# Kernel optimization log

Hardware: AMD Instinct MI355X
Metric: run time of the kernel (lower is better)

## Reference

```python
import jax, jax.numpy as jnp
import numpy as np

B, N, P, H, E, M, O, T = 4, 128, 512, 64, 32, 64, 64, 64

def _normalize(v, axis=-1, eps=1e-12):
    n = jnp.sqrt(jnp.sum(v * v, axis=axis, keepdims=True))
    return v / jnp.maximum(n, eps)

def _quat_mul(a, b):
    aw, ax, ay, az = a[..., 0], a[..., 1], a[..., 2], a[..., 3]
    bw, bx, by, bz = b[..., 0], b[..., 1], b[..., 2], b[..., 3]
    return jnp.stack([
        aw*bw - ax*bx - ay*by - az*bz,
        aw*bx + ax*bw + ay*bz - az*by,
        aw*by - ax*bz + ay*bw + az*bx,
        aw*bz + ax*by - ay*bx + az*bw], axis=-1)

def _quat_conj(q):
    return q * jnp.array([1.0, -1.0, -1.0, -1.0], dtype=q.dtype)

def _quat_rotate(q, v):
    # rotate vectors v [...,3] by unit quaternions q [...,4] in (w,x,y,z)
    qv = q[..., 1:]
    w = q[..., :1]
    t = 2.0 * jnp.cross(qv, v)
    return v + w * t + jnp.cross(qv, t)

def _mlp(x, W1, b1, W2, b2):
    return jax.nn.relu(x @ W1 + b1) @ W2 + b2

def setup_inputs():
    key = jax.random.key(0)
    ks = jax.random.split(key, 20)
    def w(k, i, o):
        return (jax.random.normal(k, (i, o), jnp.float32) / np.sqrt(i)).astype(jnp.float32)
    inp = dict(
        q=_normalize(jax.random.normal(ks[0], (B, N, 4), jnp.float32)),
        x=jax.random.normal(ks[1], (B, N, 3), jnp.float32),
        torsions=jax.random.normal(ks[2], (B, N, 7, 2), jnp.float32),
        h=jax.random.normal(ks[3], (B, N, H), jnp.float32),
        e=jax.random.normal(ks[4], (B, N, N, E), jnp.float32),
        node_mask=jnp.ones((B, N), bool),
        pocket_q=_normalize(jax.random.normal(ks[5], (B, P, 4), jnp.float32)),
        pocket_x=jax.random.normal(ks[6], (B, P, 3), jnp.float32),
        pocket_e=jax.random.normal(ks[7], (B, N, P, E), jnp.float32),
        pocket_h=jax.random.normal(ks[8], (B, P, H), jnp.float32),
        pocket_mask=jnp.ones((B, P), bool),
        Wm1=w(ks[9], 2 * H + E + 9, T), bm1=jnp.zeros((T,), jnp.float32),
        Wm2=w(ks[10], T, M), bm2=jnp.zeros((M,), jnp.float32),
        Wf1=w(ks[11], H + M, T), bf1=jnp.zeros((T,), jnp.float32),
        Wf2=w(ks[12], T, O), bf2=jnp.zeros((O,), jnp.float32),
        Wx1=w(ks[13], M, T), bx1=jnp.zeros((T,), jnp.float32),
        Wx2=w(ks[14], T, 3), bx2=jnp.zeros((3,), jnp.float32),
        Wq1=w(ks[15], M, T), bq1=jnp.zeros((T,), jnp.float32),
        Wq2=w(ks[16], T, 4), bq2=jnp.zeros((4,), jnp.float32),
        Wt1=w(ks[17], M, T), bt1=jnp.zeros((T,), jnp.float32),
        Wt2=w(ks[18], T, 14), bt2=jnp.zeros((14,), jnp.float32),
    )
    return inp

def _forward(q, x, torsions, h, e, pocket_q, pocket_x, pocket_e, pocket_h,
             node_mask, pocket_mask,
             Wm1, bm1, Wm2, bm2, Wf1, bf1, Wf2, bf2,
             Wx1, bx1, Wx2, bx2, Wq1, bq1, Wq2, bq2, Wt1, bt1, Wt2, bt2):
    b, n, hd = h.shape
    p = pocket_h.shape[-2]
    eye = jnp.eye(n, dtype=bool)
    pep_mm = node_mask[:, :, None] & node_mask[:, None, :] & (~eye)[None]
    poc_mm = node_mask[:, :, None] & pocket_mask[:, None, :]
    msg_mask = jnp.concatenate([pep_mm, poc_mm], axis=-1).astype(h.dtype)  # [B,N,N+P]
    n_neigh = (node_mask.sum(-1) + pocket_mask.sum(-1) - 1).astype(h.dtype)

    all_x = jnp.concatenate([x, pocket_x], axis=-2)   # [B,N+P,3]
    all_q = jnp.concatenate([q, pocket_q], axis=-2)   # [B,N+P,4]

    diff = x[:, :, None, :] - all_x[:, None, :, :]    # [B,N,N+P,3]
    d2 = jnp.sum(diff * diff, axis=-1)                # [B,N,N+P] == cat(peptide_d2, pocket_d2)
    qdot = jnp.abs(jnp.sum(q[:, :, None, :] * all_q[:, None, :, :], axis=-1))
    conj_j = _quat_conj(all_q)[:, None, :, :]         # inverse of frame j rotation
    local_x = _quat_rotate(conj_j, diff)              # R_j^T (x_i - x_j): global_to_local.apply
    local_q = _quat_mul(conj_j, q[:, :, None, :])     # q_j^{-1} * q_i

    hi = jnp.broadcast_to(h[:, :, None, :], (b, n, n + p, hd))
    hj = jnp.broadcast_to(jnp.concatenate([h, pocket_h], axis=-2)[:, None, :, :], (b, n, n + p, hd))
    e_all = jnp.concatenate([e, pocket_e], axis=-2)

    feat = jnp.concatenate([hi, hj, e_all, local_x, local_q, d2[..., None], qdot[..., None]], axis=-1)
    m = _mlp(feat, Wm1, bm1, Wm2, bm2) * msg_mask[..., None]
    msum = m.sum(axis=-2)                             # [B,N,M]

    o = _mlp(jnp.concatenate([h, msum], axis=-1), Wf1, bf1, Wf2, bf2)
    upd_torsions = _normalize(_mlp(msum, Wt1, bt1, Wt2, bt2).reshape(torsions.shape))

    dx = _mlp(m, Wx1, bx1, Wx2, bx2) * msg_mask[..., None]
    dq = _mlp(msum, Wq1, bq1, Wq2, bq2)
    ident = jnp.array([1.0, 0.0, 0.0, 0.0], dtype=dq.dtype)
    dq = jnp.where(node_mask[..., None], dq, ident)
    dq = _normalize(dq)
    upd_q = _quat_mul(q, dq)
    upd_q = jnp.where(node_mask[..., None], upd_q, ident)
    upd_q = _normalize(upd_q)                         # Rigid(Rotation(..., normalize_quats=True))

    rot_j = _normalize(all_q)[:, None, :, :]          # local->global rotation, normalize_quats=True
    upd_x = x + _quat_rotate(rot_j, dx).sum(axis=-2) / n_neigh[:, None, None]
    return upd_q, upd_x, upd_torsions, o

def reference(q, x, torsions, h, e, node_mask, pocket_q, pocket_x, pocket_e, pocket_h, pocket_mask,
              Wm1, bm1, Wm2, bm2, Wf1, bf1, Wf2, bf2,
              Wx1, bx1, Wx2, bx2, Wq1, bq1, Wq2, bq2, Wt1, bt1, Wt2, bt2):
    return _forward(q, x, torsions, h, e, pocket_q, pocket_x, pocket_e, pocket_h,
                    node_mask, pocket_mask,
                    Wm1, bm1, Wm2, bm2, Wf1, bf1, Wf2, bf2,
                    Wx1, bx1, Wx2, bx2, Wq1, bq1, Wq2, bq2, Wt1, bt1, Wt2, bt2)
```

## Files before the change

### kernel.cpp

```cpp
#include <hip/hip_runtime.h>
#include <stdint.h>

#define NB 4
#define NN 128
#define NP 512
#define NJ 640
#define HD 64
#define ED 32
#define NW 8

typedef unsigned short u16;
typedef __attribute__((ext_vector_type(8))) short short8;
typedef __attribute__((ext_vector_type(4))) float f32x4;

#define OFF_Q 0
#define OFF_X 2048
#define OFF_T 3584
#define OFF_O 10752

__device__ __forceinline__ uint32_t cvtpk(float a, float b) {
  uint32_t r;
  asm("v_cvt_pk_bf16_f32 %0, %1, %2" : "=v"(r) : "v"(a), "v"(b));
  return r;
}
__device__ __forceinline__ u16 bfh(float a) { return (u16)cvtpk(a, 0.f); }

__device__ __forceinline__ int w1row64(int k) {
  if (k < 32) return 128 + k;
  if (k < 35) return 160 + (k - 32);
  if (k < 39) return 163 + (k - 35);
  if (k == 39) return 167;
  if (k == 40) return 168;
  return -1;
}

__global__ void __launch_bounds__(256)
hj_pre(const float* __restrict__ h, const float* __restrict__ ph,
       const float* __restrict__ Wm1, float* __restrict__ HjW) {
  const int r = blockIdx.x * 4 + (threadIdx.x >> 6);
  const int lane = threadIdx.x & 63;
  const int b = r / NJ, j = r - b * NJ;
  const float* hr = (j < NN) ? h + ((size_t)(b * NN + j)) * HD
                             : ph + ((size_t)(b * NP + (j - NN))) * HD;
  float hv = hr[lane];
  float acc = 0.f;
#pragma unroll 16
  for (int k = 0; k < 64; ++k)
    acc += __shfl(hv, k) * Wm1[(size_t)(64 + k) * 64 + lane];
  HjW[(size_t)r * 64 + lane] = acc;
}

__global__ void __launch_bounds__(512, 2)
egnn_fused(const float* __restrict__ q, const float* __restrict__ x,
           const float* __restrict__ h, const float* __restrict__ e,
           const float* __restrict__ pe, const float* __restrict__ pq,
           const float* __restrict__ px, const float* __restrict__ ph,
           const float* __restrict__ HjW,
           const float* __restrict__ Wm1, const float* __restrict__ bm1,
           const float* __restrict__ Wm2, const float* __restrict__ bm2,
           const float* __restrict__ Wx1, const float* __restrict__ bx1,
           const float* __restrict__ Wx2, const float* __restrict__ bx2,
           const float* __restrict__ Wf1, const float* __restrict__ bf1,
           const float* __restrict__ Wf2, const float* __restrict__ bf2_,
           const float* __restrict__ Wq1, const float* __restrict__ bq1,
           const float* __restrict__ Wq2, const float* __restrict__ bq2,
           const float* __restrict__ Wt1, const float* __restrict__ bt1,
           const float* __restrict__ Wt2, const float* __restrict__ bt2,
           float* __restrict__ out)
{
  __shared__ __align__(16) u16 sW1B[64 * 64];
  __shared__ __align__(16) u16 sW2B[64 * 64];
  __shared__ __align__(16) u16 sWx1B[64 * 64];
  __shared__ __align__(16) u16 sWx2B[16 * 64];
  __shared__ __align__(16) u16 sF[NW][16 * 64];
  __shared__ __align__(16) u16 sT[NW][16 * 64];
  __shared__ float sDxT[NW][16][3];
  __shared__ float sMsum[NW][64];
  __shared__ float sDx[NW][3];
  __shared__ float sHiP[64];

  const int b = blockIdx.x >> 7;
  const int i = blockIdx.x & 127;
  const int tid = threadIdx.x;
  const int wid = tid >> 6;
  const int lane = tid & 63;
  const int nl = lane & 15;
  const int quad = lane >> 4;
  const size_t node = (size_t)(b * NN + i);

  u16* sFw = sF[wid];
  u16* sTw = sT[wid];

  const int er = lane >> 2, ec = lane & 3;

  float4 EA, EB;
  {
    int jr = wid * 16 + er;
    const float* eb = (jr < NN)
        ? e + ((node * NN) + jr) * ED + ec * 8
        : pe + ((node * NP) + (jr - NN)) * ED + ec * 8;
    EA = *(const float4*)eb;
    EB = *(const float4*)(eb + 4);
  }

  for (int idx = tid; idx < 64 * 64; idx += 512) {
    int n = idx >> 6, k = idx & 63;
    int ks = k ^ ((n & 7) << 3);
    int row = w1row64(k);
    sW1B[n * 64 + ks]  = (row < 0) ? (u16)0 : bfh(Wm1[(size_t)row * 64 + n]);
    sW2B[n * 64 + ks]  = bfh(Wm2[(size_t)k * 64 + n]);
    sWx1B[n * 64 + ks] = bfh(Wx1[(size_t)k * 64 + n]);
  }
  for (int idx = tid; idx < 16 * 64; idx += 512) {
    int n = idx >> 6, k = idx & 63;
    sWx2B[n * 64 + (k ^ ((n & 7) << 3))] =
        (n < 3) ? bfh(Wx2[(size_t)k * 3 + n]) : (u16)0;
  }
  for (int idx = lane; idx < 16 * 64 / 2; idx += 64) ((uint32_t*)sFw)[idx] = 0;

  if (tid >= 64 && tid < 128) {
    int col = tid - 64;
    float acc = bm1[col];
#pragma unroll 8
    for (int k = 0; k < HD; ++k) acc += h[node * HD + k] * Wm1[k * 64 + col];
    sHiP[col] = acc;
  }

  const float* qr0 = q + node * 4;
  const float qi0 = qr0[0], qi1 = qr0[1], qi2 = qr0[2], qi3 = qr0[3];
  const float* xr0 = x + node * 3;
  const float xi0 = xr0[0], xi1 = xr0[1], xi2 = xr0[2];

  __syncthreads();

  float HiF[4], bm2F[4], bx1F[4];
#pragma unroll
  for (int nt = 0; nt < 4; ++nt) {
    HiF[nt] = sHiP[nt * 16 + nl];
    bm2F[nt] = bm2[nt * 16 + nl];
    bx1F[nt] = bx1[nt * 16 + nl];
  }
  const float bx2F = (nl < 3) ? bx2[nl] : 0.f;

  f32x4 msum[4];
#pragma unroll
  for (int nt = 0; nt < 4; ++nt) msum[nt] = (f32x4){0.f, 0.f, 0.f, 0.f};
  float dxs0 = 0.f, dxs1 = 0.f, dxs2 = 0.f;

  const int swr = (nl & 7) << 3;
  const float* HjB = HjW + (size_t)b * NJ * 64;

  for (int tl = wid; tl < 40; tl += NW) {
    const int jb = tl * 16;

    float hj[4][4];
#pragma unroll
    for (int r = 0; r < 4; ++r)
#pragma unroll
      for (int nt = 0; nt < 4; ++nt)
        hj[r][nt] = HjB[(size_t)(jb + quad * 4 + r) * 64 + nt * 16 + nl];

    float4 qj;
    float xj0 = 0.f, xj1 = 0.f, xj2 = 0.f;
    if (lane < 16) {
      int j = jb + lane;
      const float* qr = (j < NN) ? q + ((size_t)(b * NN + j)) * 4
                                 : pq + ((size_t)(b * NP + (j - NN))) * 4;
      qj = *(const float4*)qr;
      const float* xr = (j < NN) ? x + ((size_t)(b * NN + j)) * 3
                                 : px + ((size_t)(b * NP + (j - NN))) * 3;
      xj0 = xr[0]; xj1 = xr[1]; xj2 = xr[2];
    }

    {
      const int sw = (er & 7) << 3;
      uint4 pw;
      pw.x = cvtpk(EA.x, EA.y); pw.y = cvtpk(EA.z, EA.w);
      pw.z = cvtpk(EB.x, EB.y); pw.w = cvtpk(EB.z, EB.w);
      *(uint4*)&sFw[er * 64 + ((ec * 8) ^ sw)] = pw;
    }
    if (tl + NW < 40) {
      int jr2 = (tl + NW) * 16 + er;
      const float* eb = (jr2 < NN)
          ? e + ((node * NN) + jr2) * ED + ec * 8
          : pe + ((node * NP) + (jr2 - NN)) * ED + ec * 8;
      EA = *(const float4*)eb;
      EB = *(const float4*)(eb + 4);
    }

    float nqw = 0.f, nqx = 0.f, nqy = 0.f, nqz = 0.f;
    if (lane < 16) {
      float d0 = xi0 - xj0, d1 = xi1 - xj1, d2v = xi2 - xj2;
      float d2 = d0 * d0 + d1 * d1 + d2v * d2v;
      float qdot = fabsf(qi0 * qj.x + qi1 * qj.y + qi2 * qj.z + qi3 * qj.w);
      float ajw = qj.x, ajx = -qj.y, ajy = -qj.z, ajz = -qj.w;
      float t0 = 2.f * (ajy * d2v - ajz * d1);
      float t1 = 2.f * (ajz * d0 - ajx * d2v);
      float t2 = 2.f * (ajx * d1 - ajy * d0);
      float lx0 = d0 + ajw * t0 + (ajy * t2 - ajz * t1);
      float lx1 = d1 + ajw * t1 + (ajz * t0 - ajx * t2);
      float lx2 = d2v + ajw * t2 + (ajx * t1 - ajy * t0);
      float lqw = ajw * qi0 - ajx * qi1 - ajy * qi2 - ajz * qi3;
      float lqx = ajw * qi1 + ajx * qi0 + ajy * qi3 - ajz * qi2;
      float lqy = ajw * qi2 - ajx * qi3 + ajy * qi0 + ajz * qi1;
      float lqz = ajw * qi3 + ajx * qi2 - ajy * qi1 + ajz * qi0;
      float nn2 = qj.x * qj.x + qj.y * qj.y + qj.z * qj.z + qj.w * qj.w;
      float rn = 1.f / fmaxf(sqrtf(nn2), 1e-12f);
      nqw = qj.x * rn; nqx = qj.y * rn; nqy = qj.z * rn; nqz = qj.w * rn;
      uint4 g0, g1;
      g0.x = cvtpk(lx0, lx1); g0.y = cvtpk(lx2, lqw);
      g0.z = cvtpk(lqx, lqy); g0.w = cvtpk(lqz, d2);
      g1.x = cvtpk(qdot, 0.f); g1.y = 0; g1.z = 0; g1.w = 0;
      const int sw = (lane & 7) << 3;
      *(uint4*)&sFw[lane * 64 + (32 ^ sw)] = g0;
      *(uint4*)&sFw[lane * 64 + (40 ^ sw)] = g1;
    }

    f32x4 acc[4];
#pragma unroll
    for (int nt = 0; nt < 4; ++nt)
      acc[nt] = (f32x4){HiF[nt] + hj[0][nt], HiF[nt] + hj[1][nt],
                        HiF[nt] + hj[2][nt], HiF[nt] + hj[3][nt]};
#pragma unroll
    for (int ks = 0; ks < 2; ++ks) {
      const int ko = (ks * 32 + quad * 8) ^ swr;
      short8 af = *(const short8*)&sFw[nl * 64 + ko];
#pragma unroll
      for (int nt = 0; nt < 4; ++nt) {
        short8 bfr = *(const short8*)&sW1B[(nt * 16 + nl) * 64 + ko];
        acc[nt] = __builtin_amdgcn_mfma_f32_16x16x32_bf16(af, bfr, acc[nt], 0, 0, 0);
      }
    }
#pragma unroll
    for (int r = 0; r < 4; ++r) {
      const int row = quad * 4 + r;
      const int sw2 = (row & 7) << 3;
#pragma unroll
      for (int nt = 0; nt < 4; ++nt)
        sTw[row * 64 + ((nt * 16 + nl) ^ sw2)] = bfh(fmaxf(acc[nt][r], 0.f));
    }

#pragma unroll
    for (int nt = 0; nt < 4; ++nt)
      acc[nt] = (f32x4){bm2F[nt], bm2F[nt], bm2F[nt], bm2F[nt]};
#pragma unroll
    for (int ks = 0; ks < 2; ++ks) {
      const int ko = (ks * 32 + quad * 8) ^ swr;
      short8 af = *(const short8*)&sTw[nl * 64 + ko];
#pragma unroll
      for (int nt = 0; nt < 4; ++nt) {
        short8 bfr = *(const short8*)&sW2B[(nt * 16 + nl) * 64 + ko];
        acc[nt] = __builtin_amdgcn_mfma_f32_16x16x32_bf16(af, bfr, acc[nt], 0, 0, 0);
      }
    }
#pragma unroll
    for (int r = 0; r < 4; ++r) {
      const int row = quad * 4 + r;
      const int sw2 = (row & 7) << 3;
#pragma unroll
      for (int nt = 0; nt < 4; ++nt) {
        float v = acc[nt][r];
        if (jb + row == i) v = 0.f;
        msum[nt][r] += v;
        sTw[row * 64 + ((nt * 16 + nl) ^ sw2)] = bfh(v);
      }
    }

#pragma unroll
    for (int nt = 0; nt < 4; ++nt)
      acc[nt] = (f32x4){bx1F[nt], bx1F[nt], bx1F[nt], bx1F[nt]};
#pragma unroll
    for (int ks = 0; ks < 2; ++ks) {
      const int ko = (ks * 32 + quad * 8) ^ swr;
      short8 af = *(const short8*)&sTw[nl * 64 + ko];
#pragma unroll
      for (int nt = 0; nt < 4; ++nt) {
        short8 bfr = *(const short8*)&sWx1B[(nt * 16 + nl) * 64 + ko];
        acc[nt] = __builtin_amdgcn_mfma_f32_16x16x32_bf16(af, bfr, acc[nt], 0, 0, 0);
      }
    }
#pragma unroll
    for (int r = 0; r < 4; ++r) {
      const int row = quad * 4 + r;
      const int sw2 = (row & 7) << 3;
#pragma unroll
      for (int nt = 0; nt < 4; ++nt)
        sTw[row * 64 + ((nt * 16 + nl) ^ sw2)] = bfh(fmaxf(acc[nt][r], 0.f));
    }

    f32x4 dacc = (f32x4){bx2F, bx2F, bx2F, bx2F};
#pragma unroll
    for (int ks = 0; ks < 2; ++ks) {
      const int ko = (ks * 32 + quad * 8) ^ swr;
      short8 af = *(const short8*)&sTw[nl * 64 + ko];
      short8 bfr = *(const short8*)&sWx2B[nl * 64 + ko];
      dacc = __builtin_amdgcn_mfma_f32_16x16x32_bf16(af, bfr, dacc, 0, 0, 0);
    }
    if (nl < 3) {
#pragma unroll
      for (int r = 0; r < 4; ++r) sDxT[wid][quad * 4 + r][nl] = dacc[r];
    }
    if (lane < 16) {
      int j = jb + lane;
      if (j != i) {
        float dxc0 = sDxT[wid][lane][0];
        float dxc1 = sDxT[wid][lane][1];
        float dxc2 = sDxT[wid][lane][2];
        float rt0 = 2.f * (nqy * dxc2 - nqz * dxc1);
        float rt1 = 2.f * (nqz * dxc0 - nqx * dxc2);
        float rt2 = 2.f * (nqx * dxc1 - nqy * dxc0);
        dxs0 += dxc0 + nqw * rt0 + (nqy * rt2 - nqz * rt1);
        dxs1 += dxc1 + nqw * rt1 + (nqz * rt0 - nqx * rt2);
        dxs2 += dxc2 + nqw * rt2 + (nqx * rt1 - nqy * rt0);
      }
    }
  }

#pragma unroll
  for (int nt = 0; nt < 4; ++nt) {
    float s = msum[nt][0] + msum[nt][1] + msum[nt][2] + msum[nt][3];
    s += __shfl_xor(s, 16);
    s += __shfl_xor(s, 32);
    if (lane < 16) sMsum[wid][nt * 16 + lane] = s;
  }
  {
    float a = dxs0, bb = dxs1, cc = dxs2;
#pragma unroll
    for (int off = 1; off < 16; off <<= 1) {
      a += __shfl_xor(a, off);
      bb += __shfl_xor(bb, off);
      cc += __shfl_xor(cc, off);
    }
    if (lane == 0) { sDx[wid][0] = a; sDx[wid][1] = bb; sDx[wid][2] = cc; }
  }
  __syncthreads();

  float* sPh3 = (float*)sWx2B;
  if (wid == 0) {
    float ms = 0.f;
#pragma unroll
    for (int w = 0; w < NW; ++w) ms += sMsum[w][lane];
    sPh3[0 * 64 + lane] = ms;
    float f1a = bf1[lane], f1b = 0.f;
    __syncwarp();
#pragma unroll 8
    for (int k = 0; k < 64; ++k) {
      f1a += h[node * HD + k] * Wf1[k * 64 + lane];
      f1b += sPh3[0 * 64 + k] * Wf1[(64 + k) * 64 + lane];
    }
    float f1 = fmaxf(f1a + f1b, 0.f);
    __syncwarp();
    sPh3[0 * 64 + lane] = f1;
    float oacc = bf2_[lane];
    __syncwarp();
#pragma unroll 8
    for (int k = 0; k < 64; ++k) oacc += sPh3[0 * 64 + k] * Wf2[k * 64 + lane];
    out[OFF_O + node * 64 + lane] = oacc;
  } else if (wid == 1) {
    float ms = 0.f;
#pragma unroll
    for (int w = 0; w < NW; ++w) ms += sMsum[w][lane];
    sPh3[1 * 64 + lane] = ms;
    float a = bq1[lane];
    __syncwarp();
#pragma unroll 8
    for (int k = 0; k < 64; ++k) a += sPh3[1 * 64 + k] * Wq1[k * 64 + lane];
    a = fmaxf(a, 0.f);
    float p0 = a * Wq2[lane * 4 + 0];
    float p1 = a * Wq2[lane * 4 + 1];
    float p2 = a * Wq2[lane * 4 + 2];
    float p3 = a * Wq2[lane * 4 + 3];
#pragma unroll
    for (int off = 32; off >= 1; off >>= 1) {
      p0 += __shfl_xor(p0, off);
      p1 += __shfl_xor(p1, off);
      p2 += __shfl_xor(p2, off);
      p3 += __shfl_xor(p3, off);
    }
    float dq0 = p0 + bq2[0], dq1 = p1 + bq2[1];
    float dq2 = p2 + bq2[2], dq3 = p3 + bq2[3];
    float n = fmaxf(sqrtf(dq0 * dq0 + dq1 * dq1 + dq2 * dq2 + dq3 * dq3), 1e-12f);
    dq0 /= n; dq1 /= n; dq2 /= n; dq3 /= n;
    float uw = qi0 * dq0 - qi1 * dq1 - qi2 * dq2 - qi3 * dq3;
    float ux = qi0 * dq1 + qi1 * dq0 + qi2 * dq3 - qi3 * dq2;
    float uy = qi0 * dq2 - qi1 * dq3 + qi2 * dq0 + qi3 * dq1;
    float uz = qi0 * dq3 + qi1 * dq2 - qi2 * dq1 + qi3 * dq0;
    float n2 = fmaxf(sqrtf(uw * uw + ux * ux + uy * uy + uz * uz), 1e-12f);
    if (lane == 0) {
      float* po = out + OFF_Q + node * 4;
      po[0] = uw / n2; po[1] = ux / n2; po[2] = uy / n2; po[3] = uz / n2;
    }
  } else if (wid == 2) {
    float ms = 0.f;
#pragma unroll
    for (int w = 0; w < NW; ++w) ms += sMsum[w][lane];
    sPh3[2 * 64 + lane] = ms;
    float a = bt1[lane];
    __syncwarp();
#pragma unroll 8
    for (int k = 0; k < 64; ++k) a += sPh3[2 * 64 + k] * Wt1[k * 64 + lane];
    a = fmaxf(a, 0.f);
    __syncwarp();
    sPh3[2 * 64 + lane] = a;
    __syncwarp();
    if (lane < 14) {
      float v = bt2[lane];
#pragma unroll 8
      for (int k = 0; k < 64; ++k) v += sPh3[2 * 64 + k] * Wt2[k * 14 + lane];
      float pv = __shfl_xor(v, 1);
      float nrm = fmaxf(sqrtf(v * v + pv * pv), 1e-12f);
      out[OFF_T + node * 14 + lane] = v / nrm;
    }
  } else if (wid == 3) {
    if (lane < 3) {
      float xs = 0.f;
#pragma unroll
      for (int w = 0; w < NW; ++w) xs += sDx[w][lane];
      float xiv = (lane == 0) ? xi0 : (lane == 1) ? xi1 : xi2;
      out[OFF_X + node * 3 + lane] = xiv + xs / 639.0f;
    }
  }
}

extern "C" void kernel_launch(void* const* d_in, const int* in_sizes, int n_in,
                              void* d_out, int out_size, void* d_ws, size_t ws_size,
                              hipStream_t stream) {
  const float* q   = (const float*)d_in[0];
  const float* x   = (const float*)d_in[1];
  const float* h   = (const float*)d_in[3];
  const float* e   = (const float*)d_in[4];
  const float* pq  = (const float*)d_in[6];
  const float* px  = (const float*)d_in[7];
  const float* pe  = (const float*)d_in[8];
  const float* ph  = (const float*)d_in[9];
  const float* Wm1 = (const float*)d_in[11];
  const float* bm1 = (const float*)d_in[12];
  const float* Wm2 = (const float*)d_in[13];
  const float* bm2 = (const float*)d_in[14];
  const float* Wf1 = (const float*)d_in[15];
  const float* bf1 = (const float*)d_in[16];
  const float* Wf2 = (const float*)d_in[17];
  const float* bf2_ = (const float*)d_in[18];
  const float* Wx1 = (const float*)d_in[19];
  const float* bx1 = (const float*)d_in[20];
  const float* Wx2 = (const float*)d_in[21];
  const float* bx2 = (const float*)d_in[22];
  const float* Wq1 = (const float*)d_in[23];
  const float* bq1 = (const float*)d_in[24];
  const float* Wq2 = (const float*)d_in[25];
  const float* bq2 = (const float*)d_in[26];
  const float* Wt1 = (const float*)d_in[27];
  const float* bt1 = (const float*)d_in[28];
  const float* Wt2 = (const float*)d_in[29];
  const float* bt2 = (const float*)d_in[30];

  float* HjW = (float*)d_ws;

  hj_pre<<<NB * NJ / 4, 256, 0, stream>>>(h, ph, Wm1, HjW);
  egnn_fused<<<NB * NN, 512, 0, stream>>>(
      q, x, h, e, pe, pq, px, ph, HjW,
      Wm1, bm1, Wm2, bm2, Wx1, bx1, Wx2, bx2,
      Wf1, bf1, Wf2, bf2_, Wq1, bq1, Wq2, bq2,
      Wt1, bt1, Wt2, bt2, (float*)d_out);
}
```

Baseline: 190.4 us.

## Shrink shared memory and retile HjW layout to raise occupancy to four blocks

Merges the per-warp feature and temp LDS buffers into one, keeps Wx2 as register fragments instead of shared memory, and aliases the dx and message-sum scratch, so that four 512-thread blocks can share a CU (launch bounds raised from 2 to 4). The HjW precompute is written in a tiled, transposed layout so each lane can fetch its hj values with four float4 loads instead of sixteen scalar loads. The cost is tighter register limits under the new launch bound, with a risk of spills, and more reuse of a single LDS buffer across consecutive stages within a warp.

```diff
diff --git a/kernel.cpp b/kernel.cpp
--- a/kernel.cpp
+++ b/kernel.cpp
@@ -47,10 +47,10 @@
 #pragma unroll 16
   for (int k = 0; k < 64; ++k)
     acc += __shfl(hv, k) * Wm1[(size_t)(64 + k) * 64 + lane];
-  HjW[(size_t)r * 64 + lane] = acc;
+  HjW[((size_t)(b * 40 + (j >> 4))) * 1024 + lane * 16 + (j & 15)] = acc;
 }
 
-__global__ void __launch_bounds__(512, 2)
+__global__ void __launch_bounds__(512, 4)
 egnn_fused(const float* __restrict__ q, const float* __restrict__ x,
            const float* __restrict__ h, const float* __restrict__ e,
            const float* __restrict__ pe, const float* __restrict__ pq,
@@ -71,11 +71,8 @@
   __shared__ __align__(16) u16 sW1B[64 * 64];
   __shared__ __align__(16) u16 sW2B[64 * 64];
   __shared__ __align__(16) u16 sWx1B[64 * 64];
-  __shared__ __align__(16) u16 sWx2B[16 * 64];
-  __shared__ __align__(16) u16 sF[NW][16 * 64];
-  __shared__ __align__(16) u16 sT[NW][16 * 64];
-  __shared__ float sDxT[NW][16][3];
-  __shared__ float sMsum[NW][64];
+  __shared__ __align__(16) u16 sB[NW][16 * 64];
+  __shared__ float sRed[NW][64];
   __shared__ float sDx[NW][3];
   __shared__ float sHiP[64];
 
@@ -88,8 +85,8 @@
   const int quad = lane >> 4;
   const size_t node = (size_t)(b * NN + i);
 
-  u16* sFw = sF[wid];
-  u16* sTw = sT[wid];
+  u16* sBw = sB[wid];
+  float* sDxTw = sRed[wid];
 
   const int er = lane >> 2, ec = lane & 3;
 
@@ -111,12 +108,7 @@
     sW2B[n * 64 + ks]  = bfh(Wm2[(size_t)k * 64 + n]);
     sWx1B[n * 64 + ks] = bfh(Wx1[(size_t)k * 64 + n]);
   }
-  for (int idx = tid; idx < 16 * 64; idx += 512) {
-    int n = idx >> 6, k = idx & 63;
-    sWx2B[n * 64 + (k ^ ((n & 7) << 3))] =
-        (n < 3) ? bfh(Wx2[(size_t)k * 3 + n]) : (u16)0;
-  }
-  for (int idx = lane; idx < 16 * 64 / 2; idx += 64) ((uint32_t*)sFw)[idx] = 0;
+  for (int idx = lane; idx < 16 * 64 / 2; idx += 64) ((uint32_t*)sBw)[idx] = 0;
 
   if (tid >= 64 && tid < 128) {
     int col = tid - 64;
@@ -131,6 +123,19 @@
   const float* xr0 = x + node * 3;
   const float xi0 = xr0[0], xi1 = xr0[1], xi2 = xr0[2];
 
+  short8 Wx2f[2];
+#pragma unroll
+  for (int ks = 0; ks < 2; ++ks) {
+    const int k0 = ks * 32 + quad * 8;
+    float v[8];
+#pragma unroll
+    for (int r = 0; r < 8; ++r) v[r] = (nl < 3) ? Wx2[(size_t)(k0 + r) * 3 + nl] : 0.f;
+    union { uint32_t u[4]; short8 s; } cv;
+    cv.u[0] = cvtpk(v[0], v[1]); cv.u[1] = cvtpk(v[2], v[3]);
+    cv.u[2] = cvtpk(v[4], v[5]); cv.u[3] = cvtpk(v[6], v[7]);
+    Wx2f[ks] = cv.s;
+  }
+
   __syncthreads();
 
   float HiF[4], bm2F[4], bx1F[4];
@@ -148,17 +153,15 @@
   float dxs0 = 0.f, dxs1 = 0.f, dxs2 = 0.f;
 
   const int swr = (nl & 7) << 3;
-  const float* HjB = HjW + (size_t)b * NJ * 64;
 
   for (int tl = wid; tl < 40; tl += NW) {
     const int jb = tl * 16;
 
-    float hj[4][4];
-#pragma unroll
-    for (int r = 0; r < 4; ++r)
-#pragma unroll
-      for (int nt = 0; nt < 4; ++nt)
-        hj[r][nt] = HjB[(size_t)(jb + quad * 4 + r) * 64 + nt * 16 + nl];
+    const float* HjT = HjW + ((size_t)(b * 40 + tl)) * 1024;
+    float4 hjv[4];
+#pragma unroll
+    for (int nt = 0; nt < 4; ++nt)
+      hjv[nt] = *(const float4*)&HjT[(nt * 16 + nl) * 16 + quad * 4];
 
     float4 qj;
     float xj0 = 0.f, xj1 = 0.f, xj2 = 0.f;
@@ -177,7 +180,7 @@
       uint4 pw;
       pw.x = cvtpk(EA.x, EA.y); pw.y = cvtpk(EA.z, EA.w);
       pw.z = cvtpk(EB.x, EB.y); pw.w = cvtpk(EB.z, EB.w);
-      *(uint4*)&sFw[er * 64 + ((ec * 8) ^ sw)] = pw;
+      *(uint4*)&sBw[er * 64 + ((ec * 8) ^ sw)] = pw;
     }
     if (tl + NW < 40) {
       int jr2 = (tl + NW) * 16 + er;
@@ -212,19 +215,19 @@
       g0.z = cvtpk(lqx, lqy); g0.w = cvtpk(lqz, d2);
       g1.x = cvtpk(qdot, 0.f); g1.y = 0; g1.z = 0; g1.w = 0;
       const int sw = (lane & 7) << 3;
-      *(uint4*)&sFw[lane * 64 + (32 ^ sw)] = g0;
-      *(uint4*)&sFw[lane * 64 + (40 ^ sw)] = g1;
+      *(uint4*)&sBw[lane * 64 + (32 ^ sw)] = g0;
+      *(uint4*)&sBw[lane * 64 + (40 ^ sw)] = g1;
     }
 
     f32x4 acc[4];
 #pragma unroll
     for (int nt = 0; nt < 4; ++nt)
-      acc[nt] = (f32x4){HiF[nt] + hj[0][nt], HiF[nt] + hj[1][nt],
-                        HiF[nt] + hj[2][nt], HiF[nt] + hj[3][nt]};
+      acc[nt] = (f32x4){HiF[nt] + hjv[nt].x, HiF[nt] + hjv[nt].y,
+                        HiF[nt] + hjv[nt].z, HiF[nt] + hjv[nt].w};
 #pragma unroll
     for (int ks = 0; ks < 2; ++ks) {
       const int ko = (ks * 32 + quad * 8) ^ swr;
-      short8 af = *(const short8*)&sFw[nl * 64 + ko];
+      short8 af = *(const short8*)&sBw[nl * 64 + ko];
 #pragma unroll
       for (int nt = 0; nt < 4; ++nt) {
         short8 bfr = *(const short8*)&sW1B[(nt * 16 + nl) * 64 + ko];
@@ -237,7 +240,7 @@
       const int sw2 = (row & 7) << 3;
 #pragma unroll
       for (int nt = 0; nt < 4; ++nt)
-        sTw[row * 64 + ((nt * 16 + nl) ^ sw2)] = bfh(fmaxf(acc[nt][r], 0.f));
+        sBw[row * 64 + ((nt * 16 + nl) ^ sw2)] = bfh(fmaxf(acc[nt][r], 0.f));
     }
 
 #pragma unroll
@@ -246,7 +249,7 @@
 #pragma unroll
     for (int ks = 0; ks < 2; ++ks) {
       const int ko = (ks * 32 + quad * 8) ^ swr;
-      short8 af = *(const short8*)&sTw[nl * 64 + ko];
+      short8 af = *(const short8*)&sBw[nl * 64 + ko];
 #pragma unroll
       for (int nt = 0; nt < 4; ++nt) {
         short8 bfr = *(const short8*)&sW2B[(nt * 16 + nl) * 64 + ko];
@@ -262,7 +265,7 @@
         float v = acc[nt][r];
         if (jb + row == i) v = 0.f;
         msum[nt][r] += v;
-        sTw[row * 64 + ((nt * 16 + nl) ^ sw2)] = bfh(v);
+        sBw[row * 64 + ((nt * 16 + nl) ^ sw2)] = bfh(v);
       }
     }
 
@@ -272,7 +275,7 @@
 #pragma unroll
     for (int ks = 0; ks < 2; ++ks) {
       const int ko = (ks * 32 + quad * 8) ^ swr;
-      short8 af = *(const short8*)&sTw[nl * 64 + ko];
+      short8 af = *(const short8*)&sBw[nl * 64 + ko];
 #pragma unroll
       for (int nt = 0; nt < 4; ++nt) {
         short8 bfr = *(const short8*)&sWx1B[(nt * 16 + nl) * 64 + ko];
@@ -285,27 +288,26 @@
       const int sw2 = (row & 7) << 3;
 #pragma unroll
       for (int nt = 0; nt < 4; ++nt)
-        sTw[row * 64 + ((nt * 16 + nl) ^ sw2)] = bfh(fmaxf(acc[nt][r], 0.f));
+        sBw[row * 64 + ((nt * 16 + nl) ^ sw2)] = bfh(fmaxf(acc[nt][r], 0.f));
     }
 
     f32x4 dacc = (f32x4){bx2F, bx2F, bx2F, bx2F};
 #pragma unroll
     for (int ks = 0; ks < 2; ++ks) {
       const int ko = (ks * 32 + quad * 8) ^ swr;
-      short8 af = *(const short8*)&sTw[nl * 64 + ko];
-      short8 bfr = *(const short8*)&sWx2B[nl * 64 + ko];
-      dacc = __builtin_amdgcn_mfma_f32_16x16x32_bf16(af, bfr, dacc, 0, 0, 0);
+      short8 af = *(const short8*)&sBw[nl * 64 + ko];
+      dacc = __builtin_amdgcn_mfma_f32_16x16x32_bf16(af, Wx2f[ks], dacc, 0, 0, 0);
     }
     if (nl < 3) {
 #pragma unroll
-      for (int r = 0; r < 4; ++r) sDxT[wid][quad * 4 + r][nl] = dacc[r];
+      for (int r = 0; r < 4; ++r) sDxTw[(quad * 4 + r) * 3 + nl] = dacc[r];
     }
     if (lane < 16) {
       int j = jb + lane;
       if (j != i) {
-        float dxc0 = sDxT[wid][lane][0];
-        float dxc1 = sDxT[wid][lane][1];
-        float dxc2 = sDxT[wid][lane][2];
+        float dxc0 = sDxTw[lane * 3 + 0];
+        float dxc1 = sDxTw[lane * 3 + 1];
+        float dxc2 = sDxTw[lane * 3 + 2];
         float rt0 = 2.f * (nqy * dxc2 - nqz * dxc1);
         float rt1 = 2.f * (nqz * dxc0 - nqx * dxc2);
         float rt2 = 2.f * (nqx * dxc1 - nqy * dxc0);
@@ -321,7 +323,7 @@
     float s = msum[nt][0] + msum[nt][1] + msum[nt][2] + msum[nt][3];
     s += __shfl_xor(s, 16);
     s += __shfl_xor(s, 32);
-    if (lane < 16) sMsum[wid][nt * 16 + lane] = s;
+    if (lane < 16) sRed[wid][nt * 16 + lane] = s;
   }
   {
     float a = dxs0, bb = dxs1, cc = dxs2;
@@ -335,11 +337,11 @@
   }
   __syncthreads();
 
-  float* sPh3 = (float*)sWx2B;
+  float* sPh3 = (float*)sB;
   if (wid == 0) {
     float ms = 0.f;
 #pragma unroll
-    for (int w = 0; w < NW; ++w) ms += sMsum[w][lane];
+    for (int w = 0; w < NW; ++w) ms += sRed[w][lane];
     sPh3[0 * 64 + lane] = ms;
     float f1a = bf1[lane], f1b = 0.f;
     __syncwarp();
@@ -359,7 +361,7 @@
   } else if (wid == 1) {
     float ms = 0.f;
 #pragma unroll
-    for (int w = 0; w < NW; ++w) ms += sMsum[w][lane];
+    for (int w = 0; w < NW; ++w) ms += sRed[w][lane];
     sPh3[1 * 64 + lane] = ms;
     float a = bq1[lane];
     __syncwarp();
@@ -393,7 +395,7 @@
   } else if (wid == 2) {
     float ms = 0.f;
 #pragma unroll
-    for (int w = 0; w < NW; ++w) ms += sMsum[w][lane];
+    for (int w = 0; w < NW; ++w) ms += sRed[w][lane];
     sPh3[2 * 64 + lane] = ms;
     float a = bt1[lane];
     __syncwarp();
```

Result: slower. 220.2 us (+15.6%).
